# Performance work log

Hardware: AMD Instinct MI355X
Metric: run time of the kernel (lower is better)

The kernel has to match this reference:

```python
import jax, jax.numpy as jnp
import numpy as np

EPS = 1e-5
BS, NA, NC, NL, NPTS, ED, NG = 1, 900, 6, 4, 13, 256, 8
GD = ED // NG
IMG_W, IMG_H = 704.0, 256.0
FMAP_HW = [(64, 176), (32, 88), (16, 44), (8, 22)]


def _ln(x, g, b):
    m = x.mean(-1, keepdims=True)
    v = ((x - m) ** 2).mean(-1, keepdims=True)
    return (x - m) / jnp.sqrt(v + EPS) * g + b


def _grid_sample(img, grid):
    # img: [N,C,H,W]; grid: [N,P,Q,2] in [-1,1]; bilinear, zeros padding, align_corners=False
    N, C, H, W = img.shape
    gx = jnp.clip((grid[..., 0] + 1.0) * (W * 0.5) - 0.5, -1e4, 1e4)
    gy = jnp.clip((grid[..., 1] + 1.0) * (H * 0.5) - 0.5, -1e4, 1e4)
    x0 = jnp.floor(gx); y0 = jnp.floor(gy)
    wx1 = gx - x0; wy1 = gy - y0; wx0 = 1.0 - wx1; wy0 = 1.0 - wy1
    x0i = x0.astype(jnp.int32); y0i = y0.astype(jnp.int32)
    flat = img.reshape(N, C, H * W)

    def corner(xi, yi, wgt):
        valid = (xi >= 0) & (xi < W) & (yi >= 0) & (yi < H)
        idx = (jnp.clip(yi, 0, H - 1) * W + jnp.clip(xi, 0, W - 1))
        g = jax.vmap(lambda f, i: f[:, i])(flat, idx.reshape(N, -1))  # [N,C,P*Q]
        g = g.reshape(N, C, idx.shape[1], idx.shape[2])
        return g * (wgt * valid)[:, None]

    return (corner(x0i, y0i, wx0 * wy0) + corner(x0i + 1, y0i, wx1 * wy0)
            + corner(x0i, y0i + 1, wx0 * wy1) + corner(x0i + 1, y0i + 1, wx1 * wy1))


def setup_inputs() -> dict:
    key = jax.random.key(0)
    ks = jax.random.split(key, 20)
    d = {}
    d['instance_feature'] = jax.random.normal(ks[0], (BS, NA, ED), jnp.float32)
    xyz = jax.random.normal(ks[1], (BS, NA, 3), jnp.float32) * 1.5
    size = jax.random.normal(ks[2], (BS, NA, 3), jnp.float32) * 0.3
    theta = jax.random.uniform(ks[3], (BS, NA, 1), jnp.float32) * (2.0 * np.pi)
    vel = jax.random.normal(ks[4], (BS, NA, 3), jnp.float32) * 0.1
    d['anchor'] = jnp.concatenate([xyz, size, jnp.sin(theta), jnp.cos(theta), vel], -1)
    d['anchor_embed'] = jax.random.normal(ks[5], (BS, NA, ED), jnp.float32)
    for i, (h, w) in enumerate(FMAP_HW):
        d[f'fmap{i}'] = jax.random.normal(ks[6 + i], (BS, NC, ED, h, w), jnp.float32)
    base = jnp.array([[80., 0., 0., 352.], [0., 80., 0., 128.],
                      [0., 0., 0., 1.], [0., 0., 0., 1.]], jnp.float32)
    proj = jnp.tile(base, (BS, NC, 1, 1))
    proj = proj.at[:, :, :2, :].add(jax.random.normal(ks[10], (BS, NC, 2, 4), jnp.float32) * 2.0)
    d['projection_mat'] = proj
    d['image_wh'] = jnp.broadcast_to(jnp.array([IMG_W, IMG_H], jnp.float32), (BS, NC, 2))
    d['fix_scale'] = jnp.array([[0, 0, 0], [0.45, 0, 0], [-0.45, 0, 0], [0, 0.45, 0],
                                [0, -0.45, 0], [0, 0, 0.45], [0, 0, -0.45]], jnp.float32)

    def w(k, shape):
        return jax.random.normal(k, shape, jnp.float32) * 0.02

    d['lfc_w'] = w(ks[11], (ED, 6 * 3)); d['lfc_b'] = jnp.zeros((18,), jnp.float32)
    d['cam_w1'] = w(ks[12], (12, ED)); d['cam_b1'] = jnp.zeros((ED,), jnp.float32)
    d['cam_g1'] = jnp.ones((ED,), jnp.float32); d['cam_be1'] = jnp.zeros((ED,), jnp.float32)
    d['cam_w2'] = w(ks[13], (ED, ED)); d['cam_b2'] = jnp.zeros((ED,), jnp.float32)
    d['cam_g2'] = jnp.ones((ED,), jnp.float32); d['cam_be2'] = jnp.zeros((ED,), jnp.float32)
    d['wfc_w'] = w(ks[14], (ED, NG * NL * NPTS)); d['wfc_b'] = jnp.zeros((NG * NL * NPTS,), jnp.float32)
    d['op_w'] = w(ks[15], (ED, ED)); d['op_b'] = jnp.zeros((ED,), jnp.float32)
    return d


def reference(instance_feature, anchor, anchor_embed, fmap0, fmap1, fmap2, fmap3,
              projection_mat, image_wh, fix_scale, lfc_w, lfc_b,
              cam_w1, cam_b1, cam_g1, cam_be1, cam_w2, cam_b2, cam_g2, cam_be2,
              wfc_w, wfc_b, op_w, op_b):
    bs, na = instance_feature.shape[:2]
    # ---- keypoint generation ----
    size = jnp.exp(anchor[..., None, 3:6])                       # [bs,na,1,3]
    kp = fix_scale * size                                        # [bs,na,7,3]
    ls = jax.nn.sigmoid(instance_feature @ lfc_w + lfc_b).reshape(bs, na, -1, 3) - 0.5
    kp = jnp.concatenate([kp, ls * size], axis=-2)               # [bs,na,NPTS,3]
    sin, cos = anchor[..., 6:7], anchor[..., 7:8]                # [bs,na,1]
    kx, ky, kz = kp[..., 0], kp[..., 1], kp[..., 2]
    key_points = jnp.stack([cos * kx - sin * ky, sin * kx + cos * ky, kz], -1) \
                 + anchor[..., None, 0:3]                        # [bs,na,NPTS,3]
    # ---- per-cam/level/point group weights ----
    feat = instance_feature + anchor_embed
    cam_in = projection_mat[:, :, :3].reshape(bs, NC, 12)
    h = jax.nn.relu(cam_in @ cam_w1 + cam_b1); h = _ln(h, cam_g1, cam_be1)
    h = jax.nn.relu(h @ cam_w2 + cam_b2); cam_embed = _ln(h, cam_g2, cam_be2)
    f = feat[:, :, None] + cam_embed[:, None]                    # [bs,na,NC,ED]
    wts = (f @ wfc_w + wfc_b).reshape(bs, na, NC * NL * NPTS, NG)
    wts = jax.nn.softmax(wts, axis=-2).reshape(bs, na, NC, NL, NPTS, NG)
    # ---- multi-cam projection + bilinear sampling ----
    pts = jnp.concatenate([key_points, jnp.ones_like(key_points[..., :1])], -1)
    p2d = jnp.einsum('bcij,banj->bcani', projection_mat, pts)    # [bs,NC,na,NPTS,4]
    p2d = p2d[..., :2] / jnp.maximum(p2d[..., 2:3], 1e-5)
    p2d = p2d / image_wh[:, :, None, None]
    grid = (p2d * 2.0 - 1.0).reshape(bs * NC, na, NPTS, 2)
    feats = jnp.stack([_grid_sample(fm.reshape(bs * NC, ED, fm.shape[-2], fm.shape[-1]), grid)
                       for fm in (fmap0, fmap1, fmap2, fmap3)], axis=1)  # [bs*NC,NL,ED,na,NPTS]
    feats = feats.reshape(bs, NC, NL, ED, na, NPTS).transpose(0, 4, 1, 2, 5, 3)  # [bs,na,NC,NL,NPTS,ED]
    # ---- group-weighted fusion over cams & levels, then sum over points ----
    fg = feats.reshape(bs, na, NC, NL, NPTS, NG, GD)
    fused = jnp.einsum('bnclpg,bnclpgd->bnpgd', wts, fg).reshape(bs, na, NPTS, ED)
    fused = fused.sum(axis=2)                                    # [bs,na,ED]
    out = fused @ op_w + op_b
    return jnp.concatenate([out, instance_feature], axis=-1)     # [bs,na,2*ED]
```

## Files before the change

### kernel.cpp

```cpp
#include <hip/hip_runtime.h>
#include <stdint.h>

#define NA 900
#define NC 6
#define NL 4
#define NPTS 13
#define ED 256
#define NG 8
#define LNEPS 1e-5f
#define NSTAGE 718303
#define NSTAGE_BLOCKS 2806
#define NTRANS 5616
#define NCOPY 672
#define NSAMP 312

struct PIn { const void* p[24]; };

__device__ __forceinline__ float b2f(unsigned short u){
  union { uint32_t i; float f; } v; v.i = ((uint32_t)u)<<16; return v.f;
}
__device__ __forceinline__ unsigned short f2b(float f){
  union { float f; uint32_t i; } v; v.f = f;
  uint32_t r = v.i + 0x7FFFu + ((v.i>>16)&1u);
  return (unsigned short)(r>>16);
}
#define BLO(u) __uint_as_float((u)<<16)
#define BHI(u) __uint_as_float((u)&0xffff0000u)

__device__ __forceinline__ float ldx(const void* p, int i, bool bf){
  return bf ? b2f(((const unsigned short*)p)[i]) : ((const float*)p)[i];
}

__device__ __forceinline__ bool sniff_bf(const unsigned short* __restrict__ u16){
  int lane = threadIdx.x & 63;
  unsigned short u = u16[2*lane];
  int e = (u>>7)&0xFF;
  int sane = (e>=110 && e<=135) ? 1 : 0;
  #pragma unroll
  for (int m=32;m;m>>=1) sane += __shfl_xor(sane, m);
  return sane >= 48;
}

__device__ __forceinline__ void blockReduce2(float& a, float& b, float* lds){
  #pragma unroll
  for (int m=32;m;m>>=1){ a += __shfl_xor(a,m); b += __shfl_xor(b,m); }
  int w = threadIdx.x>>6;
  if ((threadIdx.x&63)==0){ lds[w]=a; lds[w+4]=b; }
  __syncthreads();
  a = lds[0]+lds[1]+lds[2]+lds[3];
  b = lds[4]+lds[5]+lds[6]+lds[7];
  __syncthreads();
}

__global__ __launch_bounds__(256) void k_prep(PIn in, float* __restrict__ stage,
                                              unsigned short* __restrict__ tf,
                                              unsigned short* __restrict__ wfcw_h,
                                              unsigned short* __restrict__ opw_h,
                                              float* __restrict__ Bc){
  const bool bf = sniff_bf((const unsigned short*)in.p[0]);
  const int tid = threadIdx.x;
  int b = blockIdx.x;

  __shared__ unsigned short T[64][68];
  __shared__ float h[ED];
  __shared__ float cE[ED];
  __shared__ float red8[8];
  __shared__ float part[4][64];

  if (b < NSTAGE_BLOCKS){
    const int cum[21] = {0,230400,240300,470700,470796,470808,470829,475437,475455,
                         478527,478783,479039,479295,544831,545087,545343,545599,
                         652095,652511,718047,718303};
    const int map[20] = {0,1,2,7,8,9,10,11,12,13,14,15,16,17,18,19,20,21,22,23};
    int idx = b*256 + tid;
    if (idx >= NSTAGE) return;
    int seg = 0, base = 0;
    #pragma unroll
    for (int s=1;s<20;s++) if (idx >= cum[s]){ seg = s; base = cum[s]; }
    const void* src = in.p[map[0]];
    #pragma unroll
    for (int s=1;s<20;s++) if (seg==s) src = in.p[map[s]];
    stage[idx] = ldx(src, idx - base, bf);
    return;
  }
  b -= NSTAGE_BLOCKS;
  if (b < NTRANS){
    const int xb[4]  = {176,44,11,3};
    const int HWs[4] = {11264,2816,704,176};
    const int TFO[4] = {0,17301504,21626880,22708224};
    int l, local;
    if      (b < 4224){ l=0; local=b;      }
    else if (b < 5280){ l=1; local=b-4224; }
    else if (b < 5544){ l=2; local=b-5280; }
    else              { l=3; local=b-5544; }
    int pt = local % xb[l]; int rest = local / xb[l];
    int ct = rest & 3; int c = rest >> 2;
    const int HW = HWs[l];
    const int px0 = pt*64;
    const void* src = in.p[3+l];
    #pragma unroll
    for (int p=0;p<2;p++){
      int lch = p*32 + (tid>>3);
      int gch = ct*64 + lch;
      int pxv = (tid&7)*8;
      size_t base = (size_t)(c*ED+gch)*HW + px0 + pxv;
      unsigned short v[8];
      if (px0 + pxv + 8 <= HW){
        if (bf){
          uint4 q = *reinterpret_cast<const uint4*>((const unsigned short*)src + base);
          v[0]=q.x&0xffff; v[1]=q.x>>16; v[2]=q.y&0xffff; v[3]=q.y>>16;
          v[4]=q.z&0xffff; v[5]=q.z>>16; v[6]=q.w&0xffff; v[7]=q.w>>16;
        } else {
          float4 f0 = *reinterpret_cast<const float4*>((const float*)src + base);
          float4 f1 = *reinterpret_cast<const float4*>((const float*)src + base + 4);
          v[0]=f2b(f0.x); v[1]=f2b(f0.y); v[2]=f2b(f0.z); v[3]=f2b(f0.w);
          v[4]=f2b(f1.x); v[5]=f2b(f1.y); v[6]=f2b(f1.z); v[7]=f2b(f1.w);
        }
      } else {
        #pragma unroll
        for (int i=0;i<8;i++){
          int px = px0+pxv+i;
          v[i] = (px<HW) ? (bf ? ((const unsigned short*)src)[base+i]
                               : f2b(((const float*)src)[base+i])) : (unsigned short)0;
        }
      }
      #pragma unroll
      for (int i=0;i<8;i++) T[pxv+i][lch] = v[i];
    }
    __syncthreads();
    unsigned short* dst = tf + TFO[l] + (size_t)c*HW*ED + ct*64;
    #pragma unroll
    for (int p=0;p<2;p++){
      int pxl = p*32 + (tid>>3);
      int px = px0 + pxl;
      if (px >= HW) continue;
      int ch8 = (tid&7)*8;
      ushort4 lo = *reinterpret_cast<ushort4*>(&T[pxl][ch8]);
      ushort4 hi = *reinterpret_cast<ushort4*>(&T[pxl][ch8+4]);
      union { ushort4 hh[2]; uint4 q; } u;
      u.hh[0]=lo; u.hh[1]=hi;
      *reinterpret_cast<uint4*>(dst + (size_t)px*ED + ch8) = u.q;
    }
    return;
  }
  b -= NTRANS;
  if (b < NCOPY){
    int idx = b*256 + tid;
    if (idx < 106496){
      wfcw_h[idx] = bf ? ((const unsigned short*)in.p[20])[idx]
                       : f2b(((const float*)in.p[20])[idx]);
    } else {
      int j = idx - 106496;
      opw_h[j] = bf ? ((const unsigned short*)in.p[22])[j]
                    : f2b(((const float*)in.p[22])[j]);
    }
    return;
  }
  b -= NCOPY;
  {
    const void* proj = in.p[7];
    const void* w1 = in.p[12]; const void* b1 = in.p[13];
    const void* g1 = in.p[14]; const void* be1 = in.p[15];
    const void* w2 = in.p[16]; const void* b2 = in.p[17];
    const void* g2 = in.p[18]; const void* be2 = in.p[19];
    const void* wfcw = in.p[20]; const void* wfcb = in.p[21];
    const int c = b/7, colt = b - (b/7)*7;
    float ci[12];
    #pragma unroll
    for (int i=0;i<12;i++) ci[i] = ldx(proj, c*16+i, bf);
    float acc = ldx(b1, tid, bf);
    #pragma unroll
    for (int k=0;k<12;k++) acc += ci[k]*ldx(w1, k*ED+tid, bf);
    float x = fmaxf(acc, 0.f);
    float s=x, q=x*x;
    blockReduce2(s,q,red8);
    float mean = s*(1.f/ED), var = q*(1.f/ED)-mean*mean;
    h[tid] = (x-mean)*rsqrtf(var+LNEPS)*ldx(g1,tid,bf) + ldx(be1,tid,bf);
    __syncthreads();
    acc = ldx(b2, tid, bf);
    #pragma unroll 8
    for (int k=0;k<ED;k++) acc += h[k]*ldx(w2, k*ED+tid, bf);
    x = fmaxf(acc,0.f);
    s=x; q=x*x;
    blockReduce2(s,q,red8);
    mean = s*(1.f/ED); var = q*(1.f/ED)-mean*mean;
    cE[tid] = (x-mean)*rsqrtf(var+LNEPS)*ldx(g2,tid,bf) + ldx(be2,tid,bf);
    __syncthreads();
    const int kc = tid>>6, colL = tid&63, col = colt*64+colL;
    float a = 0.f;
    if (col < 416){
      #pragma unroll 8
      for (int k=0;k<64;k++) a += cE[kc*64+k]*ldx(wfcw, (kc*64+k)*416+col, bf);
    }
    part[kc][colL] = a;
    __syncthreads();
    if (kc==0 && col<416)
      Bc[c*416+col] = part[0][colL]+part[1][colL]+part[2][colL]+part[3][colL] + ldx(wfcb,col,bf);
  }
}

__global__ __launch_bounds__(256) void k_anchor(
    const float* __restrict__ stage, const unsigned short* __restrict__ tf,
    const unsigned short* __restrict__ wfcw_h, const unsigned short* __restrict__ opw_h,
    const float* __restrict__ Bc, const void* __restrict__ rawinst,
    void* __restrict__ outv){
  const int n = blockIdx.x, tid = threadIdx.x;
  const bool bf = sniff_bf((const unsigned short*)rawinst);

  const float* s_inst = stage + 0;
  const float* s_anc  = stage + 230400;
  const float* s_ae   = stage + 240300;
  const float* s_proj = stage + 470700;
  const float* s_imwh = stage + 470796;
  const float* s_fixs = stage + 470808;
  const float* s_lw   = stage + 470829;
  const float* s_lb   = stage + 475437;
  const float* s_opb  = stage + 718047;

  __shared__ float ifs[ED];
  __shared__ float fe[ED];
  __shared__ float lg[NC*416];
  __shared__ uint4 cbi[NSAMP];
  __shared__ uint4 cwf[NSAMP];
  __shared__ unsigned short coff[NSAMP];
  __shared__ float red[8][ED+4];
  __shared__ float fu[ED];
  __shared__ float kp[13][3];
  __shared__ float sc[8];
  __shared__ float lsv[18];
  __shared__ int scnt;

  {
    if (tid==0) scnt = 0;
    float iv = s_inst[n*ED+tid];
    ifs[tid] = iv;
    fe[tid]  = iv + s_ae[n*ED+tid];
    if (tid < 3)       sc[tid] = s_anc[n*11+tid];
    else if (tid == 3) sc[3]   = s_anc[n*11+6];
    else if (tid == 4) sc[4]   = s_anc[n*11+7];
    else if (tid < 8)  sc[tid] = __expf(s_anc[n*11+tid-2]);
  }
  __syncthreads();
  if (tid < 144){
    int d = tid>>3, j = tid&7;
    float a = 0.f;
    #pragma unroll 8
    for (int k=j*32;k<j*32+32;k++) a += ifs[k]*s_lw[k*18+d];
    a += __shfl_xor(a,1); a += __shfl_xor(a,2); a += __shfl_xor(a,4);
    if (j==0){
      a += s_lb[d];
      lsv[d] = 1.f/(1.f+__expf(-a)) - 0.5f;
    }
  }
  __syncthreads();
  if (tid < 13){
    float kx,ky,kz;
    if (tid < 7){
      kx = s_fixs[tid*3+0]*sc[5];
      ky = s_fixs[tid*3+1]*sc[6];
      kz = s_fixs[tid*3+2]*sc[7];
    } else {
      int j = tid-7;
      kx = lsv[j*3+0]*sc[5]; ky = lsv[j*3+1]*sc[6]; kz = lsv[j*3+2]*sc[7];
    }
    kp[tid][0] = sc[4]*kx - sc[3]*ky + sc[0];
    kp[tid][1] = sc[3]*kx + sc[4]*ky + sc[1];
    kp[tid][2] = kz + sc[2];
  }
  {
    int col2 = (tid < 160) ? tid+256 : 415;
    float a0 = 0.f, a1 = 0.f;
    #pragma unroll 4
    for (int k=0;k<ED;k++){
      float fv = fe[k];
      a0 += fv*b2f(wfcw_h[k*416+tid]);
      a1 += fv*b2f(wfcw_h[k*416+col2]);
    }
    #pragma unroll
    for (int c=0;c<NC;c++){
      lg[c*416+tid] = a0 + Bc[c*416+tid];
      if (tid < 160) lg[c*416+tid+256] = a1 + Bc[c*416+tid+256];
    }
  }
  __syncthreads();
  #pragma unroll
  for (int pass=0;pass<2;pass++){
    int s = tid + pass*256;
    if (s < NSAMP){
      int c = s/52, rr = s - c*52;
      int l = rr/13, p = rr - l*13;
      float m[12];
      #pragma unroll
      for (int i=0;i<12;i++) m[i] = s_proj[c*16+i];
      float X=kp[p][0], Y=kp[p][1], Z=kp[p][2];
      float x = m[0]*X + m[1]*Y + m[2]*Z  + m[3];
      float y = m[4]*X + m[5]*Y + m[6]*Z  + m[7];
      float z = m[8]*X + m[9]*Y + m[10]*Z + m[11];
      float d = fmaxf(z, 1e-5f);
      float px = x/(d*s_imwh[c*2+0]), py = y/(d*s_imwh[c*2+1]);
      const int W = 176>>l, H = 64>>l;
      const int TFO[4] = {0,17301504,21626880,22708224};
      float gx = fminf(fmaxf(px*(float)W - 0.5f, -10000.f), 10000.f);
      float gy = fminf(fmaxf(py*(float)H - 0.5f, -10000.f), 10000.f);
      float xf = floorf(gx), yf = floorf(gy);
      int x0 = (int)xf, y0 = (int)yf;
      float wx1 = gx-xf, wy1 = gy-yf;
      float wx0 = 1.f-wx1, wy0 = 1.f-wy1;
      bool vx0 = (x0>=0)&&(x0<W),   vx1 = (x0+1>=0)&&(x0+1<W);
      bool vy0 = (y0>=0)&&(y0<H),   vy1 = (y0+1>=0)&&(y0+1<H);
      float w00 = (vx0&&vy0) ? wx0*wy0 : 0.f;
      float w10 = (vx1&&vy0) ? wx1*wy0 : 0.f;
      float w01 = (vx0&&vy1) ? wx0*wy1 : 0.f;
      float w11 = (vx1&&vy1) ? wx1*wy1 : 0.f;
      if (w00+w10+w01+w11 != 0.f){
        int cx0 = min(max(x0,0),W-1), cx1 = min(max(x0+1,0),W-1);
        int cy0 = min(max(y0,0),H-1), cy1 = min(max(y0+1,0),H-1);
        uint32_t cam = (uint32_t)TFO[l] + (uint32_t)(c*H*W)*ED;
        uint4 bi, wv;
        bi.x = cam + (uint32_t)(cy0*W+cx0)*ED;
        bi.y = cam + (uint32_t)(cy0*W+cx1)*ED;
        bi.z = cam + (uint32_t)(cy1*W+cx0)*ED;
        bi.w = cam + (uint32_t)(cy1*W+cx1)*ED;
        wv.x = __float_as_uint(w00); wv.y = __float_as_uint(w10);
        wv.z = __float_as_uint(w01); wv.w = __float_as_uint(w11);
        int slot = atomicAdd(&scnt, 1);
        cbi[slot] = bi;
        cwf[slot] = wv;
        coff[slot] = (unsigned short)(c*416 + rr*8);
      }
    }
  }
  {
    const int g = tid>>5, j = tid&31;
    float v[10]; float m = -1e30f;
    #pragma unroll
    for (int i=0;i<10;i++){
      int e = j + 32*i;
      float val = -1e30f;
      if (e < NSAMP){
        int c = e/52, rr = e - c*52;
        val = lg[c*416 + rr*8 + g];
        m = fmaxf(m, val);
      }
      v[i] = val;
    }
    #pragma unroll
    for (int mk=16;mk;mk>>=1) m = fmaxf(m, __shfl_xor(m, mk, 32));
    float sum = 0.f;
    #pragma unroll
    for (int i=0;i<10;i++){
      if (j + 32*i < NSAMP){ float ex = __expf(v[i]-m); v[i] = ex; sum += ex; }
    }
    #pragma unroll
    for (int mk=16;mk;mk>>=1) sum += __shfl_xor(sum, mk, 32);
    float inv = 1.f/sum;
    #pragma unroll
    for (int i=0;i<10;i++){
      int e = j + 32*i;
      if (e < NSAMP){
        int c = e/52, rr = e - c*52;
        lg[c*416 + rr*8 + g] = v[i]*inv;
      }
    }
  }
  __syncthreads();
  {
    const int m = scnt;
    const int strm = tid>>5, lane32 = tid&31;
    const int ch8 = lane32*8, gg = lane32>>2;
    float acc[8] = {0,0,0,0,0,0,0,0};
    int i = strm;
    for (; i + 8 < m; i += 16){
      uint4 biA = cbi[i],   wfA = cwf[i];
      uint4 biB = cbi[i+8], wfB = cwf[i+8];
      float wgA = lg[coff[i]+gg],  wgB = lg[coff[i+8]+gg];
      uint4 a00 = *reinterpret_cast<const uint4*>(tf + biA.x + ch8);
      uint4 a10 = *reinterpret_cast<const uint4*>(tf + biA.y + ch8);
      uint4 a01 = *reinterpret_cast<const uint4*>(tf + biA.z + ch8);
      uint4 a11 = *reinterpret_cast<const uint4*>(tf + biA.w + ch8);
      uint4 b00 = *reinterpret_cast<const uint4*>(tf + biB.x + ch8);
      uint4 b10 = *reinterpret_cast<const uint4*>(tf + biB.y + ch8);
      uint4 b01 = *reinterpret_cast<const uint4*>(tf + biB.z + ch8);
      uint4 b11 = *reinterpret_cast<const uint4*>(tf + biB.w + ch8);
      float pA00 = wgA*__uint_as_float(wfA.x), pA10 = wgA*__uint_as_float(wfA.y);
      float pA01 = wgA*__uint_as_float(wfA.z), pA11 = wgA*__uint_as_float(wfA.w);
      float pB00 = wgB*__uint_as_float(wfB.x), pB10 = wgB*__uint_as_float(wfB.y);
      float pB01 = wgB*__uint_as_float(wfB.z), pB11 = wgB*__uint_as_float(wfB.w);
      acc[0] += pA00*BLO(a00.x)+pA10*BLO(a10.x)+pA01*BLO(a01.x)+pA11*BLO(a11.x)
              + pB00*BLO(b00.x)+pB10*BLO(b10.x)+pB01*BLO(b01.x)+pB11*BLO(b11.x);
      acc[1] += pA00*BHI(a00.x)+pA10*BHI(a10.x)+pA01*BHI(a01.x)+pA11*BHI(a11.x)
              + pB00*BHI(b00.x)+pB10*BHI(b10.x)+pB01*BHI(b01.x)+pB11*BHI(b11.x);
      acc[2] += pA00*BLO(a00.y)+pA10*BLO(a10.y)+pA01*BLO(a01.y)+pA11*BLO(a11.y)
              + pB00*BLO(b00.y)+pB10*BLO(b10.y)+pB01*BLO(b01.y)+pB11*BLO(b11.y);
      acc[3] += pA00*BHI(a00.y)+pA10*BHI(a10.y)+pA01*BHI(a01.y)+pA11*BHI(a11.y)
              + pB00*BHI(b00.y)+pB10*BHI(b10.y)+pB01*BHI(b01.y)+pB11*BHI(b11.y);
      acc[4] += pA00*BLO(a00.z)+pA10*BLO(a10.z)+pA01*BLO(a01.z)+pA11*BLO(a11.z)
              + pB00*BLO(b00.z)+pB10*BLO(b10.z)+pB01*BLO(b01.z)+pB11*BLO(b11.z);
      acc[5] += pA00*BHI(a00.z)+pA10*BHI(a10.z)+pA01*BHI(a01.z)+pA11*BHI(a11.z)
              + pB00*BHI(b00.z)+pB10*BHI(b10.z)+pB01*BHI(b01.z)+pB11*BHI(b11.z);
      acc[6] += pA00*BLO(a00.w)+pA10*BLO(a10.w)+pA01*BLO(a01.w)+pA11*BLO(a11.w)
              + pB00*BLO(b00.w)+pB10*BLO(b10.w)+pB01*BLO(b01.w)+pB11*BLO(b11.w);
      acc[7] += pA00*BHI(a00.w)+pA10*BHI(a10.w)+pA01*BHI(a01.w)+pA11*BHI(a11.w)
              + pB00*BHI(b00.w)+pB10*BHI(b10.w)+pB01*BHI(b01.w)+pB11*BHI(b11.w);
    }
    for (; i < m; i += 8){
      uint4 bi = cbi[i], wf = cwf[i];
      float wg = lg[coff[i]+gg];
      uint4 q00 = *reinterpret_cast<const uint4*>(tf + bi.x + ch8);
      uint4 q10 = *reinterpret_cast<const uint4*>(tf + bi.y + ch8);
      uint4 q01 = *reinterpret_cast<const uint4*>(tf + bi.z + ch8);
      uint4 q11 = *reinterpret_cast<const uint4*>(tf + bi.w + ch8);
      float p00 = wg*__uint_as_float(wf.x), p10 = wg*__uint_as_float(wf.y);
      float p01 = wg*__uint_as_float(wf.z), p11 = wg*__uint_as_float(wf.w);
      acc[0] += p00*BLO(q00.x)+p10*BLO(q10.x)+p01*BLO(q01.x)+p11*BLO(q11.x);
      acc[1] += p00*BHI(q00.x)+p10*BHI(q10.x)+p01*BHI(q01.x)+p11*BHI(q11.x);
      acc[2] += p00*BLO(q00.y)+p10*BLO(q10.y)+p01*BLO(q01.y)+p11*BLO(q11.y);
      acc[3] += p00*BHI(q00.y)+p10*BHI(q10.y)+p01*BHI(q01.y)+p11*BHI(q11.y);
      acc[4] += p00*BLO(q00.z)+p10*BLO(q10.z)+p01*BLO(q01.z)+p11*BLO(q11.z);
      acc[5] += p00*BHI(q00.z)+p10*BHI(q10.z)+p01*BHI(q01.z)+p11*BHI(q11.z);
      acc[6] += p00*BLO(q00.w)+p10*BLO(q10.w)+p01*BLO(q01.w)+p11*BLO(q11.w);
      acc[7] += p00*BHI(q00.w)+p10*BHI(q10.w)+p01*BHI(q01.w)+p11*BHI(q11.w);
    }
    *reinterpret_cast<float4*>(&red[strm][ch8])   = make_float4(acc[0],acc[1],acc[2],acc[3]);
    *reinterpret_cast<float4*>(&red[strm][ch8+4]) = make_float4(acc[4],acc[5],acc[6],acc[7]);
  }
  __syncthreads();
  {
    float r = 0.f;
    #pragma unroll
    for (int i=0;i<8;i++) r += red[i][tid];
    fu[tid] = r;
  }
  __syncthreads();
  {
    float acc = s_opb[tid];
    #pragma unroll 4
    for (int k=0;k<ED;k++) acc += fu[k]*b2f(opw_h[k*ED+tid]);
    float pv = ifs[tid];
    if (bf){
      unsigned short* outh = (unsigned short*)outv;
      outh[n*512+tid]     = f2b(acc);
      outh[n*512+256+tid] = f2b(pv);
    } else {
      float* outf = (float*)outv;
      outf[n*512+tid]     = acc;
      outf[n*512+256+tid] = pv;
    }
  }
}

extern "C" void kernel_launch(void* const* d_in, const int* in_sizes, int n_in,
                              void* d_out, int out_size, void* d_ws, size_t ws_size,
                              hipStream_t stream){
  char* ws = (char*)d_ws;
  size_t off = 0;
  auto alloc = [&](size_t bytes)->char*{
    char* p = ws + off; off += (bytes + 63) & ~size_t(63); return p;
  };
  unsigned short* tf = (unsigned short*)alloc((size_t)22978560*2);
  float* stage  = (float*)alloc((size_t)NSTAGE*4);
  unsigned short* wfcw_h = (unsigned short*)alloc((size_t)106496*2);
  unsigned short* opw_h  = (unsigned short*)alloc((size_t)65536*2);
  float* Bc     = (float*)alloc((size_t)NC*416*4);

  PIn in;
  for (int i=0;i<24;i++) in.p[i] = d_in[i];

  k_prep<<<NSTAGE_BLOCKS + NTRANS + NCOPY + 42, 256, 0, stream>>>(in, stage, tf, wfcw_h, opw_h, Bc);
  k_anchor<<<NA, 256, 0, stream>>>(stage, tf, wfcw_h, opw_h, Bc, d_in[0], d_out);
}
```

Measured before the change: 253.1 us.

## Double k_anchor block to 512 threads and compact samples with wave ballot

```diff
diff --git a/kernel.cpp b/kernel.cpp
--- a/kernel.cpp
+++ b/kernel.cpp
@@ -199,7 +199,7 @@
   }
 }
 
-__global__ __launch_bounds__(256) void k_anchor(
+__global__ __launch_bounds__(512) void k_anchor(
     const float* __restrict__ stage, const unsigned short* __restrict__ tf,
     const unsigned short* __restrict__ wfcw_h, const unsigned short* __restrict__ opw_h,
     const float* __restrict__ Bc, const void* __restrict__ rawinst,
@@ -223,22 +223,23 @@
   __shared__ uint4 cbi[NSAMP];
   __shared__ uint4 cwf[NSAMP];
   __shared__ unsigned short coff[NSAMP];
-  __shared__ float red[8][ED+4];
+  __shared__ float red[16][ED+4];
   __shared__ float fu[ED];
   __shared__ float kp[13][3];
   __shared__ float sc[8];
   __shared__ float lsv[18];
-  __shared__ int scnt;
-
-  {
-    if (tid==0) scnt = 0;
+  __shared__ int wcnt[5];
+
+  if (tid < 256){
     float iv = s_inst[n*ED+tid];
     ifs[tid] = iv;
     fe[tid]  = iv + s_ae[n*ED+tid];
-    if (tid < 3)       sc[tid] = s_anc[n*11+tid];
-    else if (tid == 3) sc[3]   = s_anc[n*11+6];
-    else if (tid == 4) sc[4]   = s_anc[n*11+7];
-    else if (tid < 8)  sc[tid] = __expf(s_anc[n*11+tid-2]);
+  } else {
+    int t2 = tid-256;
+    if (t2 < 3)       sc[t2] = s_anc[n*11+t2];
+    else if (t2 == 3) sc[3]  = s_anc[n*11+6];
+    else if (t2 == 4) sc[4]  = s_anc[n*11+7];
+    else if (t2 < 8)  sc[t2] = __expf(s_anc[n*11+t2-2]);
   }
   __syncthreads();
   if (tid < 144){
@@ -268,74 +269,74 @@
     kp[tid][2] = kz + sc[2];
   }
   {
-    int col2 = (tid < 160) ? tid+256 : 415;
-    float a0 = 0.f, a1 = 0.f;
+    int col = (tid < 416) ? tid : 415;
+    float a0 = 0.f;
     #pragma unroll 4
-    for (int k=0;k<ED;k++){
-      float fv = fe[k];
-      a0 += fv*b2f(wfcw_h[k*416+tid]);
-      a1 += fv*b2f(wfcw_h[k*416+col2]);
-    }
-    #pragma unroll
-    for (int c=0;c<NC;c++){
-      lg[c*416+tid] = a0 + Bc[c*416+tid];
-      if (tid < 160) lg[c*416+tid+256] = a1 + Bc[c*416+tid+256];
-    }
-  }
-  __syncthreads();
-  #pragma unroll
-  for (int pass=0;pass<2;pass++){
-    int s = tid + pass*256;
-    if (s < NSAMP){
-      int c = s/52, rr = s - c*52;
-      int l = rr/13, p = rr - l*13;
-      float m[12];
+    for (int k=0;k<ED;k++) a0 += fe[k]*b2f(wfcw_h[k*416+col]);
+    if (tid < 416){
       #pragma unroll
-      for (int i=0;i<12;i++) m[i] = s_proj[c*16+i];
-      float X=kp[p][0], Y=kp[p][1], Z=kp[p][2];
-      float x = m[0]*X + m[1]*Y + m[2]*Z  + m[3];
-      float y = m[4]*X + m[5]*Y + m[6]*Z  + m[7];
-      float z = m[8]*X + m[9]*Y + m[10]*Z + m[11];
-      float d = fmaxf(z, 1e-5f);
-      float px = x/(d*s_imwh[c*2+0]), py = y/(d*s_imwh[c*2+1]);
-      const int W = 176>>l, H = 64>>l;
-      const int TFO[4] = {0,17301504,21626880,22708224};
-      float gx = fminf(fmaxf(px*(float)W - 0.5f, -10000.f), 10000.f);
-      float gy = fminf(fmaxf(py*(float)H - 0.5f, -10000.f), 10000.f);
-      float xf = floorf(gx), yf = floorf(gy);
-      int x0 = (int)xf, y0 = (int)yf;
-      float wx1 = gx-xf, wy1 = gy-yf;
-      float wx0 = 1.f-wx1, wy0 = 1.f-wy1;
-      bool vx0 = (x0>=0)&&(x0<W),   vx1 = (x0+1>=0)&&(x0+1<W);
-      bool vy0 = (y0>=0)&&(y0<H),   vy1 = (y0+1>=0)&&(y0+1<H);
-      float w00 = (vx0&&vy0) ? wx0*wy0 : 0.f;
-      float w10 = (vx1&&vy0) ? wx1*wy0 : 0.f;
-      float w01 = (vx0&&vy1) ? wx0*wy1 : 0.f;
-      float w11 = (vx1&&vy1) ? wx1*wy1 : 0.f;
-      if (w00+w10+w01+w11 != 0.f){
-        int cx0 = min(max(x0,0),W-1), cx1 = min(max(x0+1,0),W-1);
-        int cy0 = min(max(y0,0),H-1), cy1 = min(max(y0+1,0),H-1);
-        uint32_t cam = (uint32_t)TFO[l] + (uint32_t)(c*H*W)*ED;
-        uint4 bi, wv;
-        bi.x = cam + (uint32_t)(cy0*W+cx0)*ED;
-        bi.y = cam + (uint32_t)(cy0*W+cx1)*ED;
-        bi.z = cam + (uint32_t)(cy1*W+cx0)*ED;
-        bi.w = cam + (uint32_t)(cy1*W+cx1)*ED;
-        wv.x = __float_as_uint(w00); wv.y = __float_as_uint(w10);
-        wv.z = __float_as_uint(w01); wv.w = __float_as_uint(w11);
-        int slot = atomicAdd(&scnt, 1);
-        cbi[slot] = bi;
-        cwf[slot] = wv;
-        coff[slot] = (unsigned short)(c*416 + rr*8);
-      }
-    }
+      for (int c=0;c<NC;c++) lg[c*416+tid] = a0 + Bc[c*416+tid];
+    }
+  }
+  __syncthreads();
+  uint4 bi, wv; unsigned short offv = 0; bool valid = false; int pre = 0;
+  if (tid < NSAMP){
+    int c = tid/52, rr = tid - c*52;
+    int l = rr/13, p = rr - l*13;
+    float m[12];
+    #pragma unroll
+    for (int i=0;i<12;i++) m[i] = s_proj[c*16+i];
+    float X=kp[p][0], Y=kp[p][1], Z=kp[p][2];
+    float x = m[0]*X + m[1]*Y + m[2]*Z  + m[3];
+    float y = m[4]*X + m[5]*Y + m[6]*Z  + m[7];
+    float z = m[8]*X + m[9]*Y + m[10]*Z + m[11];
+    float d = fmaxf(z, 1e-5f);
+    float px = x/(d*s_imwh[c*2+0]), py = y/(d*s_imwh[c*2+1]);
+    const int W = 176>>l, H = 64>>l;
+    const int TFO[4] = {0,17301504,21626880,22708224};
+    float gx = fminf(fmaxf(px*(float)W - 0.5f, -10000.f), 10000.f);
+    float gy = fminf(fmaxf(py*(float)H - 0.5f, -10000.f), 10000.f);
+    float xf = floorf(gx), yf = floorf(gy);
+    int x0 = (int)xf, y0 = (int)yf;
+    float wx1 = gx-xf, wy1 = gy-yf;
+    float wx0 = 1.f-wx1, wy0 = 1.f-wy1;
+    bool vx0 = (x0>=0)&&(x0<W),   vx1 = (x0+1>=0)&&(x0+1<W);
+    bool vy0 = (y0>=0)&&(y0<H),   vy1 = (y0+1>=0)&&(y0+1<H);
+    float w00 = (vx0&&vy0) ? wx0*wy0 : 0.f;
+    float w10 = (vx1&&vy0) ? wx1*wy0 : 0.f;
+    float w01 = (vx0&&vy1) ? wx0*wy1 : 0.f;
+    float w11 = (vx1&&vy1) ? wx1*wy1 : 0.f;
+    valid = (w00+w10+w01+w11 != 0.f);
+    unsigned long long mb = __ballot(valid);
+    pre = __popcll(mb & ((1ull<<(tid&63))-1ull));
+    if ((tid&63)==0) wcnt[tid>>6] = __popcll(mb);
+    if (valid){
+      int cx0 = min(max(x0,0),W-1), cx1 = min(max(x0+1,0),W-1);
+      int cy0 = min(max(y0,0),H-1), cy1 = min(max(y0+1,0),H-1);
+      uint32_t cam = (uint32_t)TFO[l] + (uint32_t)(c*H*W)*ED;
+      bi.x = cam + (uint32_t)(cy0*W+cx0)*ED;
+      bi.y = cam + (uint32_t)(cy0*W+cx1)*ED;
+      bi.z = cam + (uint32_t)(cy1*W+cx0)*ED;
+      bi.w = cam + (uint32_t)(cy1*W+cx1)*ED;
+      wv.x = __float_as_uint(w00); wv.y = __float_as_uint(w10);
+      wv.z = __float_as_uint(w01); wv.w = __float_as_uint(w11);
+      offv = (unsigned short)(c*416 + rr*8);
+    }
+  }
+  __syncthreads();
+  if (valid){
+    int w = tid>>6, base = 0;
+    #pragma unroll
+    for (int i=0;i<5;i++) if (i<w) base += wcnt[i];
+    int slot = base + pre;
+    cbi[slot] = bi; cwf[slot] = wv; coff[slot] = offv;
   }
   {
-    const int g = tid>>5, j = tid&31;
-    float v[10]; float m = -1e30f;
-    #pragma unroll
-    for (int i=0;i<10;i++){
-      int e = j + 32*i;
+    const int g = tid>>6, j = tid&63;
+    float v[5]; float m = -1e30f;
+    #pragma unroll
+    for (int i=0;i<5;i++){
+      int e = j + 64*i;
       float val = -1e30f;
       if (e < NSAMP){
         int c = e/52, rr = e - c*52;
@@ -345,18 +346,18 @@
       v[i] = val;
     }
     #pragma unroll
-    for (int mk=16;mk;mk>>=1) m = fmaxf(m, __shfl_xor(m, mk, 32));
+    for (int mk=32;mk;mk>>=1) m = fmaxf(m, __shfl_xor(m, mk));
     float sum = 0.f;
     #pragma unroll
-    for (int i=0;i<10;i++){
-      if (j + 32*i < NSAMP){ float ex = __expf(v[i]-m); v[i] = ex; sum += ex; }
-    }
-    #pragma unroll
-    for (int mk=16;mk;mk>>=1) sum += __shfl_xor(sum, mk, 32);
+    for (int i=0;i<5;i++){
+      if (j + 64*i < NSAMP){ float ex = __expf(v[i]-m); v[i] = ex; sum += ex; }
+    }
+    #pragma unroll
+    for (int mk=32;mk;mk>>=1) sum += __shfl_xor(sum, mk);
     float inv = 1.f/sum;
     #pragma unroll
-    for (int i=0;i<10;i++){
-      int e = j + 32*i;
+    for (int i=0;i<5;i++){
+      int e = j + 64*i;
       if (e < NSAMP){
         int c = e/52, rr = e - c*52;
         lg[c*416 + rr*8 + g] = v[i]*inv;
@@ -365,23 +366,24 @@
   }
   __syncthreads();
   {
-    const int m = scnt;
+    const int m = wcnt[0]+wcnt[1]+wcnt[2]+wcnt[3]+wcnt[4];
     const int strm = tid>>5, lane32 = tid&31;
     const int ch8 = lane32*8, gg = lane32>>2;
+    const unsigned short* tfc = tf + ch8;
     float acc[8] = {0,0,0,0,0,0,0,0};
     int i = strm;
-    for (; i + 8 < m; i += 16){
-      uint4 biA = cbi[i],   wfA = cwf[i];
-      uint4 biB = cbi[i+8], wfB = cwf[i+8];
-      float wgA = lg[coff[i]+gg],  wgB = lg[coff[i+8]+gg];
-      uint4 a00 = *reinterpret_cast<const uint4*>(tf + biA.x + ch8);
-      uint4 a10 = *reinterpret_cast<const uint4*>(tf + biA.y + ch8);
-      uint4 a01 = *reinterpret_cast<const uint4*>(tf + biA.z + ch8);
-      uint4 a11 = *reinterpret_cast<const uint4*>(tf + biA.w + ch8);
-      uint4 b00 = *reinterpret_cast<const uint4*>(tf + biB.x + ch8);
-      uint4 b10 = *reinterpret_cast<const uint4*>(tf + biB.y + ch8);
-      uint4 b01 = *reinterpret_cast<const uint4*>(tf + biB.z + ch8);
-      uint4 b11 = *reinterpret_cast<const uint4*>(tf + biB.w + ch8);
+    for (; i + 16 < m; i += 32){
+      uint4 biA = cbi[i],    wfA = cwf[i];
+      uint4 biB = cbi[i+16], wfB = cwf[i+16];
+      float wgA = lg[coff[i]+gg],  wgB = lg[coff[i+16]+gg];
+      uint4 a00 = *reinterpret_cast<const uint4*>(tfc + biA.x);
+      uint4 a10 = *reinterpret_cast<const uint4*>(tfc + biA.y);
+      uint4 a01 = *reinterpret_cast<const uint4*>(tfc + biA.z);
+      uint4 a11 = *reinterpret_cast<const uint4*>(tfc + biA.w);
+      uint4 b00 = *reinterpret_cast<const uint4*>(tfc + biB.x);
+      uint4 b10 = *reinterpret_cast<const uint4*>(tfc + biB.y);
+      uint4 b01 = *reinterpret_cast<const uint4*>(tfc + biB.z);
+      uint4 b11 = *reinterpret_cast<const uint4*>(tfc + biB.w);
       float pA00 = wgA*__uint_as_float(wfA.x), pA10 = wgA*__uint_as_float(wfA.y);
       float pA01 = wgA*__uint_as_float(wfA.z), pA11 = wgA*__uint_as_float(wfA.w);
       float pB00 = wgB*__uint_as_float(wfB.x), pB10 = wgB*__uint_as_float(wfB.y);
@@ -403,13 +405,13 @@
       acc[7] += pA00*BHI(a00.w)+pA10*BHI(a10.w)+pA01*BHI(a01.w)+pA11*BHI(a11.w)
               + pB00*BHI(b00.w)+pB10*BHI(b10.w)+pB01*BHI(b01.w)+pB11*BHI(b11.w);
     }
-    for (; i < m; i += 8){
-      uint4 bi = cbi[i], wf = cwf[i];
+    for (; i < m; i += 16){
+      uint4 bi2 = cbi[i], wf = cwf[i];
       float wg = lg[coff[i]+gg];
-      uint4 q00 = *reinterpret_cast<const uint4*>(tf + bi.x + ch8);
-      uint4 q10 = *reinterpret_cast<const uint4*>(tf + bi.y + ch8);
-      uint4 q01 = *reinterpret_cast<const uint4*>(tf + bi.z + ch8);
-      uint4 q11 = *reinterpret_cast<const uint4*>(tf + bi.w + ch8);
+      uint4 q00 = *reinterpret_cast<const uint4*>(tfc + bi2.x);
+      uint4 q10 = *reinterpret_cast<const uint4*>(tfc + bi2.y);
+      uint4 q01 = *reinterpret_cast<const uint4*>(tfc + bi2.z);
+      uint4 q11 = *reinterpret_cast<const uint4*>(tfc + bi2.w);
       float p00 = wg*__uint_as_float(wf.x), p10 = wg*__uint_as_float(wf.y);
       float p01 = wg*__uint_as_float(wf.z), p11 = wg*__uint_as_float(wf.w);
       acc[0] += p00*BLO(q00.x)+p10*BLO(q10.x)+p01*BLO(q01.x)+p11*BLO(q11.x);
@@ -425,26 +427,32 @@
     *reinterpret_cast<float4*>(&red[strm][ch8+4]) = make_float4(acc[4],acc[5],acc[6],acc[7]);
   }
   __syncthreads();
+  if (tid < 256){
+    float r = 0.f;
+    #pragma unroll
+    for (int i=0;i<16;i++) r += red[i][tid];
+    fu[tid] = r;
+  }
+  __syncthreads();
   {
-    float r = 0.f;
-    #pragma unroll
-    for (int i=0;i<8;i++) r += red[i][tid];
-    fu[tid] = r;
-  }
-  __syncthreads();
-  {
-    float acc = s_opb[tid];
+    const int col = tid & 255, kh = tid >> 8;
+    float acc = 0.f;
     #pragma unroll 4
-    for (int k=0;k<ED;k++) acc += fu[k]*b2f(opw_h[k*ED+tid]);
-    float pv = ifs[tid];
-    if (bf){
-      unsigned short* outh = (unsigned short*)outv;
-      outh[n*512+tid]     = f2b(acc);
-      outh[n*512+256+tid] = f2b(pv);
-    } else {
-      float* outf = (float*)outv;
-      outf[n*512+tid]     = acc;
-      outf[n*512+256+tid] = pv;
+    for (int k=kh*128; k<kh*128+128; k++) acc += fu[k]*b2f(opw_h[k*ED+col]);
+    if (kh) red[0][col] = acc;
+    __syncthreads();
+    if (tid < 256){
+      float r = acc + red[0][tid] + s_opb[tid];
+      float pv = ifs[tid];
+      if (bf){
+        unsigned short* outh = (unsigned short*)outv;
+        outh[n*512+tid]     = f2b(r);
+        outh[n*512+256+tid] = f2b(pv);
+      } else {
+        float* outf = (float*)outv;
+        outf[n*512+tid]     = r;
+        outf[n*512+256+tid] = pv;
+      }
     }
   }
 }
@@ -467,5 +475,5 @@
   for (int i=0;i<24;i++) in.p[i] = d_in[i];
 
   k_prep<<<NSTAGE_BLOCKS + NTRANS + NCOPY + 42, 256, 0, stream>>>(in, stage, tf, wfcw_h, opw_h, Bc);
-  k_anchor<<<NA, 256, 0, stream>>>(stage, tf, wfcw_h, opw_h, Bc, d_in[0], d_out);
-}
+  k_anchor<<<NA, 512, 0, stream>>>(stage, tf, wfcw_h, opw_h, Bc, d_in[0], d_out);
+}
```

Result: slower. 292.7 us (+15.7%).
